# Optimization experiments

Hardware: AMD Instinct MI355X
Metric: run time of the kernel (lower is better)

The kernel has to match this reference:

```python
import jax, jax.numpy as jnp
import numpy as np

EPS_BN = 1e-5   # torch BatchNorm1d default eps
EPS_L1 = 1e-9   # offset-attention renorm eps


def batchnorm(x, g, b):
    # training-mode BN over (batch, points) per channel; x: [B, C, N]
    mu = x.mean(axis=(0, 2), keepdims=True)
    var = x.var(axis=(0, 2), keepdims=True)  # biased, matching torch normalization
    return g[None, :, None] * (x - mu) * jax.lax.rsqrt(var + EPS_BN) + b[None, :, None]


def sub_ie(x, Wqk, Wv, bv, Wt, bt, g, b):
    # x: [B, C, N]; Wqk: [C//4, C] (q_conv and k_conv share weights)
    q = jnp.einsum('dc,bcn->bdn', Wqk, x)                    # [B, C/4, N]
    energy = jnp.einsum('bdi,bdj->bij', q, q)                # [B, N, N] symmetric Gram
    att = jax.nn.softmax(energy, axis=-1)                    # softmax over keys (dim=-1)
    att = att / (EPS_L1 + att.sum(axis=1, keepdims=True))    # extra L1 renorm over queries (dim=1)
    v = jnp.einsum('dc,bcn->bdn', Wv, x) + bv[None, :, None]  # [B, C, N]
    x_r = jnp.einsum('bci,bij->bcj', v, att)                 # bmm(x_v, attention)
    y = jnp.einsum('dc,bcn->bdn', Wt, x - x_r) + bt[None, :, None]
    y = jax.nn.relu(batchnorm(y, g, b))
    return x + y


def setup_inputs() -> dict:
    key = jax.random.key(0)
    ks = jax.random.split(key, 8)
    B, Cin, C, N = 8, 64, 128, 2048
    s = lambda k, shape: jax.random.normal(k, shape, jnp.float32) * 0.05
    return {
        'x':   jax.random.normal(ks[0], (B, Cin, N), jnp.float32),
        'W1':  s(ks[1], (64, 64)),
        'g1':  jnp.ones(64, jnp.float32),  'b1': jnp.zeros(64, jnp.float32),
        'W2':  s(ks[2], (C, 64)),
        'g2':  jnp.ones(C, jnp.float32),   'b2': jnp.zeros(C, jnp.float32),
        'Wqk': s(ks[3], (4, C // 4, C)),
        'Wv':  s(ks[4], (4, C, C)),        'bv': jnp.zeros((4, C), jnp.float32),
        'Wt':  s(ks[5], (4, C, C)),        'bt': jnp.zeros((4, C), jnp.float32),
        'gn':  jnp.ones((4, C), jnp.float32), 'bnb': jnp.zeros((4, C), jnp.float32),
    }


def reference(x, W1, g1, b1, W2, g2, b2, Wqk, Wv, bv, Wt, bt, gn, bnb):
    h = jax.nn.relu(batchnorm(jnp.einsum('dc,bcn->bdn', W1, x), g1, b1))   # [B,64,N]
    h = jax.nn.relu(batchnorm(jnp.einsum('dc,bcn->bdn', W2, h), g2, b2))   # [B,128,N]
    outs = []
    for i in range(4):  # 4 structurally chained offset-attention blocks
        h = sub_ie(h, Wqk[i], Wv[i], bv[i], Wt[i], bt[i], gn[i], bnb[i])
        outs.append(h)
    return jnp.concatenate(outs, axis=1)  # [B, 512, N]
```

## Files before the change

### kernel.cpp

```cpp
#include <hip/hip_runtime.h>
#include <cstdint>
#include <cstddef>

#define NPTS 2048
#define NBAT 8

typedef unsigned long long ull;
typedef __attribute__((ext_vector_type(8))) short bf16x8;
typedef __attribute__((ext_vector_type(4))) float f32x4;

__device__ __forceinline__ float4 ld4(const float* p){ return *reinterpret_cast<const float4*>(p); }
__device__ __forceinline__ void st4(float* p, float4 v){ *reinterpret_cast<float4*>(p) = v; }
__device__ __forceinline__ unsigned short f2bf(float f){
    unsigned int u = __float_as_uint(f);
    u += 0x7FFFu + ((u >> 16) & 1u);
    return (unsigned short)(u >> 16);
}
__device__ __forceinline__ float bf2f(unsigned short h){
    return __uint_as_float(((unsigned int)h) << 16);
}

typedef __attribute__((address_space(3))) unsigned int lds_u32;
typedef __attribute__((address_space(1))) const unsigned int glb_u32;
__device__ __forceinline__ void gl2lds16(const unsigned short* g, unsigned short* l){
    __builtin_amdgcn_global_load_lds((glb_u32*)g, (lds_u32*)l, 16, 0, 0);
}

__global__ __launch_bounds__(256) void zero_kernel(float* __restrict__ p)
{
    int i = (blockIdx.x * 256 + threadIdx.x) * 4;
    st4(&p[i], (float4){0.f, 0.f, 0.f, 0.f});
}

__device__ __forceinline__ void bn_finalize(const float* part, int C, int c,
                                            float& mean, float& istd)
{
    float s = 0.f, s2 = 0.f;
    #pragma unroll
    for (int b = 0; b < NBAT; ++b) {
        s  += part[b * C + c];
        s2 += part[NBAT * C + b * C + c];
    }
    const float invn = 1.f / (NBAT * NPTS);
    mean = s * invn;
    float var = s2 * invn - mean * mean;
    istd = rsqrtf(var + 1e-5f);
}

template<int CIN, int COUT, int TD, int TN, int MODE, bool BIAS, bool BNIN, bool STATS>
__global__ __launch_bounds__(256) void lin_mfma_kernel(
        const float* __restrict__ W, const float* __restrict__ X,
        const float* __restrict__ bias,
        const float* __restrict__ gin, const float* __restrict__ betain,
        const float* __restrict__ pin, float* __restrict__ pout,
        void* __restrict__ outv, void* __restrict__ outv2)
{
    constexpr int WD  = TD / 16;
    constexpr int NPW = TN * WD / 4;
    constexpr int FB  = NPW / 16;
    constexpr int KS  = CIN / 32;
    __shared__ unsigned short Xhi[TN * CIN];
    __shared__ unsigned short Xlo[TN * CIN];
    __shared__ float gaL[CIN];
    __shared__ float beL[CIN];
    const int tid = threadIdx.x;
    const int lane = tid & 63;
    const int w = tid >> 6;
    const int g = lane >> 4;
    const int l15 = lane & 15;
    const int b = blockIdx.z;
    const int d0 = blockIdx.y * TD;
    const int n0 = blockIdx.x * TN;
    const int dw = (w % WD) * 16;
    const int nw = (w / WD) * NPW;

    if (BNIN) {
        if (tid < CIN) {
            float mean, is;
            bn_finalize(pin, CIN, tid, mean, is);
            float ga = gin[tid] * is;
            gaL[tid] = ga;
            beL[tid] = betain[tid] - mean * ga;
        }
        __syncthreads();
    }

    bf16x8 Whi[KS], Wlo[KS];
    {
        const int d = d0 + dw + l15;
        #pragma unroll
        for (int ks = 0; ks < KS; ++ks) {
            float4 a = ld4(&W[(size_t)d * CIN + ks * 32 + g * 8]);
            float4 bq = ld4(&W[(size_t)d * CIN + ks * 32 + g * 8 + 4]);
            float vv[8] = {a.x, a.y, a.z, a.w, bq.x, bq.y, bq.z, bq.w};
            bf16x8 h8, l8;
            #pragma unroll
            for (int e = 0; e < 8; ++e) {
                unsigned short hh = f2bf(vv[e]);
                h8[e] = (short)hh;
                l8[e] = (short)f2bf(vv[e] - bf2f(hh));
            }
            Whi[ks] = h8; Wlo[ks] = l8;
        }
    }
    constexpr int TN4 = TN / 4;
    constexpr int NF = (TN * CIN) / 1024;
    #pragma unroll
    for (int f = 0; f < NF; ++f) {
        int idx = tid + 256 * f;
        int c = idx / TN4;
        int n = (idx % TN4) * 4;
        float4 xv = ld4(&X[((size_t)(b * CIN + c)) * NPTS + n0 + n]);
        float vv[4] = {xv.x, xv.y, xv.z, xv.w};
        if (BNIN) {
            float ga = gaL[c], be = beL[c];
            #pragma unroll
            for (int j2 = 0; j2 < 4; ++j2) vv[j2] = fmaxf(fmaf(ga, vv[j2], be), 0.f);
        }
        #pragma unroll
        for (int j2 = 0; j2 < 4; ++j2) {
            int nn = n + j2;
            int cp = (c + nn * 8) & (CIN - 1);
            unsigned short hh = f2bf(vv[j2]);
            Xhi[nn * CIN + cp] = hh;
            Xlo[nn * CIN + cp] = f2bf(vv[j2] - bf2f(hh));
        }
    }
    __syncthreads();

    f32x4 acc[FB];
    #pragma unroll
    for (int fb = 0; fb < FB; ++fb) acc[fb] = (f32x4){0.f, 0.f, 0.f, 0.f};
    #pragma unroll
    for (int ks = 0; ks < KS; ++ks) {
        #pragma unroll
        for (int fb = 0; fb < FB; ++fb) {
            int n = nw + fb * 16 + l15;
            int cp = (ks * 32 + g * 8 + n * 8) & (CIN - 1);
            bf16x8 xh = *reinterpret_cast<bf16x8*>(&Xhi[n * CIN + cp]);
            bf16x8 xl = *reinterpret_cast<bf16x8*>(&Xlo[n * CIN + cp]);
            acc[fb] = __builtin_amdgcn_mfma_f32_16x16x32_bf16(Wlo[ks], xh, acc[fb], 0, 0, 0);
            acc[fb] = __builtin_amdgcn_mfma_f32_16x16x32_bf16(Whi[ks], xl, acc[fb], 0, 0, 0);
            acc[fb] = __builtin_amdgcn_mfma_f32_16x16x32_bf16(Whi[ks], xh, acc[fb], 0, 0, 0);
        }
    }
    const int dbase = d0 + dw + g * 4;
    float bb[4] = {0.f, 0.f, 0.f, 0.f};
    if (BIAS) {
        float4 b4 = ld4(&bias[dbase]);
        bb[0] = b4.x; bb[1] = b4.y; bb[2] = b4.z; bb[3] = b4.w;
    }
    float s1[4] = {0.f, 0.f, 0.f, 0.f};
    float s2[4] = {0.f, 0.f, 0.f, 0.f};
    #pragma unroll
    for (int fb = 0; fb < FB; ++fb) {
        int ncol = n0 + nw + fb * 16 + l15;
        if (MODE == 2) {
            unsigned short* qh = (unsigned short*)outv;
            unsigned short* ql = (unsigned short*)outv2;
            ushort4 hh, ll;
            float q0 = acc[fb][0], q1 = acc[fb][1], q2 = acc[fb][2], q3 = acc[fb][3];
            hh.x = f2bf(q0); ll.x = f2bf(q0 - bf2f(hh.x));
            hh.y = f2bf(q1); ll.y = f2bf(q1 - bf2f(hh.y));
            hh.z = f2bf(q2); ll.z = f2bf(q2 - bf2f(hh.z));
            hh.w = f2bf(q3); ll.w = f2bf(q3 - bf2f(hh.w));
            *reinterpret_cast<ushort4*>(&qh[((size_t)b * NPTS + ncol) * 32 + dbase]) = hh;
            *reinterpret_cast<ushort4*>(&ql[((size_t)b * NPTS + ncol) * 32 + dbase]) = ll;
        } else if (MODE == 1) {
            unsigned short* ob = (unsigned short*)outv;
            #pragma unroll
            for (int r = 0; r < 4; ++r)
                ob[((size_t)(b * COUT + dbase + r)) * NPTS + ncol] = f2bf(acc[fb][r] + bb[r]);
        } else {
            float* ob = (float*)outv;
            #pragma unroll
            for (int r = 0; r < 4; ++r) {
                float val = acc[fb][r] + bb[r];
                ob[((size_t)(b * COUT + dbase + r)) * NPTS + ncol] = val;
                if (STATS) { s1[r] += val; s2[r] += val * val; }
            }
        }
    }
    if (STATS) {
        #pragma unroll
        for (int r = 0; r < 4; ++r) {
            float a1 = s1[r], a2 = s2[r];
            a1 += __shfl_xor(a1, 1, 64);  a2 += __shfl_xor(a2, 1, 64);
            a1 += __shfl_xor(a1, 2, 64);  a2 += __shfl_xor(a2, 2, 64);
            a1 += __shfl_xor(a1, 4, 64);  a2 += __shfl_xor(a2, 4, 64);
            a1 += __shfl_xor(a1, 8, 64);  a2 += __shfl_xor(a2, 8, 64);
            if (l15 == 0) {
                atomicAdd(&pout[b * COUT + dbase + r], a1);
                atomicAdd(&pout[NBAT * COUT + b * COUT + dbase + r], a2);
            }
        }
    }
}

__global__ __launch_bounds__(256) void rowstats_fused_kernel(
        const unsigned short* __restrict__ qThi, const unsigned short* __restrict__ qTlo,
        float* __restrict__ rowm, float* __restrict__ rowinv)
{
    __shared__ float pm[4][16];
    __shared__ float ps[4][16];
    const int lane = threadIdx.x & 63;
    const int w = threadIdx.x >> 6;
    const int b = blockIdx.y;
    const int i0 = blockIdx.x * 16;
    const int g = lane >> 4;
    const int l15 = lane & 15;
    const int iR = i0 + l15;
    const bf16x8 bhi = *reinterpret_cast<const bf16x8*>(&qThi[((size_t)b * NPTS + iR) * 32 + g * 8]);
    const bf16x8 blo = *reinterpret_cast<const bf16x8*>(&qTlo[((size_t)b * NPTS + iR) * 32 + g * 8]);
    float m = -1e30f, s = 0.f;
    for (int t = w * 32; t < w * 32 + 32; ++t) {
        int jr = t * 16 + l15;
        const bf16x8 ahi = *reinterpret_cast<const bf16x8*>(&qThi[((size_t)b * NPTS + jr) * 32 + g * 8]);
        const bf16x8 alo = *reinterpret_cast<const bf16x8*>(&qTlo[((size_t)b * NPTS + jr) * 32 + g * 8]);
        f32x4 e4 = {0.f, 0.f, 0.f, 0.f};
        e4 = __builtin_amdgcn_mfma_f32_16x16x32_bf16(alo, bhi, e4, 0, 0, 0);
        e4 = __builtin_amdgcn_mfma_f32_16x16x32_bf16(ahi, blo, e4, 0, 0, 0);
        e4 = __builtin_amdgcn_mfma_f32_16x16x32_bf16(ahi, bhi, e4, 0, 0, 0);
        float tm = fmaxf(fmaxf(e4[0], e4[1]), fmaxf(e4[2], e4[3]));
        float nm = fmaxf(m, tm);
        s *= __expf(m - nm);
        m = nm;
        s += __expf(e4[0] - m) + __expf(e4[1] - m) + __expf(e4[2] - m) + __expf(e4[3] - m);
    }
    #pragma unroll
    for (int o = 16; o <= 32; o <<= 1) {
        float om = __shfl_xor(m, o, 64);
        float os = __shfl_xor(s, o, 64);
        float nm = fmaxf(m, om);
        s = s * __expf(m - nm) + os * __expf(om - nm);
        m = nm;
    }
    if (lane < 16) { pm[w][l15] = m; ps[w][l15] = s; }
    __syncthreads();
    if (threadIdx.x < 16) {
        float m0 = pm[0][threadIdx.x], m1 = pm[1][threadIdx.x];
        float m2 = pm[2][threadIdx.x], m3 = pm[3][threadIdx.x];
        float mf = fmaxf(fmaxf(m0, m1), fmaxf(m2, m3));
        float sf = ps[0][threadIdx.x] * __expf(m0 - mf)
                 + ps[1][threadIdx.x] * __expf(m1 - mf)
                 + ps[2][threadIdx.x] * __expf(m2 - mf)
                 + ps[3][threadIdx.x] * __expf(m3 - mf);
        rowm[(size_t)b * NPTS + i0 + threadIdx.x] = mf;
        rowinv[(size_t)b * NPTS + i0 + threadIdx.x] = 1.f / sf;
    }
}

__global__ __launch_bounds__(512) void attn_fused_kernel(
        const unsigned short* __restrict__ qThi, const unsigned short* __restrict__ qTlo,
        const unsigned short* __restrict__ V,
        const float* __restrict__ rowm, const float* __restrict__ rowinv,
        const float* __restrict__ H, float* __restrict__ T)
{
    __shared__ unsigned short Alds[128 * 128];
    __shared__ unsigned short Blds[32 * 128];
    __shared__ float cparts[8][16];
    const int tid = threadIdx.x;
    const int b  = blockIdx.y;
    const int j0 = blockIdx.x * 32;
    const int lane = tid & 63;
    const int w = tid >> 6;
    const int g = lane >> 4;
    const int l15 = lane & 15;
    const int jsub = w & 1;
    const int jl = jsub * 16 + l15;
    const int cb = (w >> 1) * 32;
    const int jb = jsub * 16;
    const bf16x8 bhi = *reinterpret_cast<const bf16x8*>(&qThi[((size_t)b * NPTS + j0 + jl) * 32 + g * 8]);
    const bf16x8 blo = *reinterpret_cast<const bf16x8*>(&qTlo[((size_t)b * NPTS + j0 + jl) * 32 + g * 8]);
    f32x4 acc[2];
    acc[0] = (f32x4){0.f, 0.f, 0.f, 0.f};
    acc[1] = (f32x4){0.f, 0.f, 0.f, 0.f};
    float csum = 0.f;

    for (int i0 = 0; i0 < NPTS; i0 += 128) {
        __syncthreads();
        #pragma unroll
        for (int t = 0; t < 4; ++t) {
            int c = w * 16 + t * 4 + g;
            int s = l15;
            int slot = (s & 8) | ((s & 7) ^ (c & 7));
            gl2lds16(V + ((size_t)(b * 128 + c)) * NPTS + i0 + slot * 8,
                     &Alds[(w * 16 + t * 4) * 128]);
        }
        #pragma unroll
        for (int half = 0; half < 2; ++half) {
            int it = (w >> 1) + half * 4;
            int iA = i0 + it * 16 + l15;
            const bf16x8 ahi = *reinterpret_cast<const bf16x8*>(&qThi[((size_t)b * NPTS + iA) * 32 + g * 8]);
            const bf16x8 alo = *reinterpret_cast<const bf16x8*>(&qTlo[((size_t)b * NPTS + iA) * 32 + g * 8]);
            f32x4 e4 = {0.f, 0.f, 0.f, 0.f};
            e4 = __builtin_amdgcn_mfma_f32_16x16x32_bf16(alo, bhi, e4, 0, 0, 0);
            e4 = __builtin_amdgcn_mfma_f32_16x16x32_bf16(ahi, blo, e4, 0, 0, 0);
            e4 = __builtin_amdgcn_mfma_f32_16x16x32_bf16(ahi, bhi, e4, 0, 0, 0);
            int ibase = i0 + it * 16 + g * 4;
            float4 mv = ld4(&rowm[(size_t)b * NPTS + ibase]);
            float4 sv = ld4(&rowinv[(size_t)b * NPTS + ibase]);
            float p0 = __expf(e4[0] - mv.x) * sv.x;
            float p1 = __expf(e4[1] - mv.y) * sv.y;
            float p2 = __expf(e4[2] - mv.z) * sv.z;
            float p3 = __expf(e4[3] - mv.w) * sv.w;
            csum += p0 + p1 + p2 + p3;
            int il = it * 16 + g * 4;
            int slot = il >> 3;
            int sl = (slot & 8) | ((slot & 7) ^ (jl & 7));
            ull pk = (ull)f2bf(p0) | ((ull)f2bf(p1) << 16) |
                     ((ull)f2bf(p2) << 32) | ((ull)f2bf(p3) << 48);
            *reinterpret_cast<ull*>(&Blds[jl * 128 + sl * 8 + (il & 7)]) = pk;
        }
        __syncthreads();
        #pragma unroll
        for (int ks = 0; ks < 4; ++ks) {
            int j = jb + l15;
            int slot = ks * 4 + g;
            int slb = (slot & 8) | ((slot & 7) ^ (j & 7));
            bf16x8 bfr = *reinterpret_cast<bf16x8*>(&Blds[j * 128 + slb * 8]);
            #pragma unroll
            for (int fa = 0; fa < 2; ++fa) {
                int c = cb + fa * 16 + l15;
                int sla = (slot & 8) | ((slot & 7) ^ (c & 7));
                bf16x8 afr = *reinterpret_cast<bf16x8*>(&Alds[c * 128 + sla * 8]);
                acc[fa] = __builtin_amdgcn_mfma_f32_16x16x32_bf16(afr, bfr, acc[fa], 0, 0, 0);
            }
        }
    }
    csum += __shfl_xor(csum, 16, 64);
    csum += __shfl_xor(csum, 32, 64);
    if (lane < 16) cparts[w][l15] = csum;
    __syncthreads();
    float cs = cparts[jsub][l15] + cparts[jsub + 2][l15]
             + cparts[jsub + 4][l15] + cparts[jsub + 6][l15];
    float inv = 1.f / (1e-9f + cs);
    int jg_ = j0 + jb + l15;
    #pragma unroll
    for (int fa = 0; fa < 2; ++fa) {
        #pragma unroll
        for (int r = 0; r < 4; ++r) {
            int c = cb + fa * 16 + g * 4 + r;
            size_t base = ((size_t)(b * 128 + c)) * NPTS + jg_;
            T[base] = H[base] - acc[fa][r] * inv;
        }
    }
}

__global__ __launch_bounds__(256) void bn_apply_kernel(const float* __restrict__ X,
        const float* __restrict__ g, const float* __restrict__ beta,
        const float* __restrict__ part, int C, float* __restrict__ out)
{
    const int bc = blockIdx.y;
    const int c = bc % C;
    const int n = blockIdx.x * 1024 + threadIdx.x * 4;
    float mean, is;
    bn_finalize(part, C, c, mean, is);
    const float ga = g[c] * is;
    const float be = beta[c] - mean * ga;
    float4 v = ld4(&X[(size_t)bc * NPTS + n]);
    float4 o;
    o.x = fmaxf(fmaf(ga, v.x, be), 0.f);
    o.y = fmaxf(fmaf(ga, v.y, be), 0.f);
    o.z = fmaxf(fmaf(ga, v.z, be), 0.f);
    o.w = fmaxf(fmaf(ga, v.w, be), 0.f);
    st4(&out[(size_t)bc * NPTS + n], o);
}

__global__ __launch_bounds__(256) void bn_res_kernel(const float* __restrict__ Y,
        const float* __restrict__ g, const float* __restrict__ beta,
        const float* __restrict__ part, float* __restrict__ H,
        float* __restrict__ out, int blk)
{
    const int bc = blockIdx.y;
    const int c = bc & 127;
    const int b = bc >> 7;
    const int n = blockIdx.x * 1024 + threadIdx.x * 4;
    float mean, is;
    bn_finalize(part, 128, c, mean, is);
    const float ga = g[c] * is;
    const float be = beta[c] - mean * ga;
    float4 yv = ld4(&Y[(size_t)bc * NPTS + n]);
    float4 hv = ld4(&H[(size_t)bc * NPTS + n]);
    float4 o;
    o.x = hv.x + fmaxf(fmaf(ga, yv.x, be), 0.f);
    o.y = hv.y + fmaxf(fmaf(ga, yv.y, be), 0.f);
    o.z = hv.z + fmaxf(fmaf(ga, yv.z, be), 0.f);
    o.w = hv.w + fmaxf(fmaf(ga, yv.w, be), 0.f);
    st4(&H[(size_t)bc * NPTS + n], o);
    st4(&out[((size_t)(b * 512 + blk * 128 + c)) * NPTS + n], o);
}

extern "C" void kernel_launch(void* const* d_in, const int* in_sizes, int n_in,
                              void* d_out, int out_size, void* d_ws, size_t ws_size,
                              hipStream_t stream)
{
    const float* x   = (const float*)d_in[0];
    const float* W1  = (const float*)d_in[1];
    const float* g1  = (const float*)d_in[2];
    const float* b1  = (const float*)d_in[3];
    const float* W2  = (const float*)d_in[4];
    const float* g2  = (const float*)d_in[5];
    const float* b2  = (const float*)d_in[6];
    const float* Wqk = (const float*)d_in[7];
    const float* Wv  = (const float*)d_in[8];
    const float* bv  = (const float*)d_in[9];
    const float* Wt  = (const float*)d_in[10];
    const float* bt  = (const float*)d_in[11];
    const float* gn  = (const float*)d_in[12];
    const float* bnb = (const float*)d_in[13];
    float* out = (float*)d_out;

    float* ws = (float*)d_ws;
    size_t off = 0;
    auto alloc = [&](size_t n) { float* p = ws + off; off += n; return p; };
    float* h      = alloc((size_t)NBAT * 128 * NPTS);
    float* t      = alloc((size_t)NBAT * 128 * NPTS);
    float* y      = alloc((size_t)NBAT * 128 * NPTS);
    float* y2     = alloc((size_t)NBAT * 128 * NPTS);
    float* part   = alloc(6 * 2 * NBAT * 128);
    float* rowm   = alloc((size_t)NBAT * NPTS);
    float* rowinv = alloc((size_t)NBAT * NPTS);
    unsigned short* vb   = (unsigned short*)alloc((size_t)NBAT * 128 * NPTS / 2);
    unsigned short* qThi = (unsigned short*)alloc((size_t)NBAT * NPTS * 32 / 2);
    unsigned short* qTlo = (unsigned short*)alloc((size_t)NBAT * NPTS * 32 / 2);
    const int PSL = 2 * NBAT * 128;

    zero_kernel<<<12, 256, 0, stream>>>(part);

    lin_mfma_kernel<64, 64, 64, 32, 0, false, false, true>
        <<<dim3(64, 1, NBAT), 256, 0, stream>>>(
        W1, x, nullptr, nullptr, nullptr, nullptr, part + 0 * PSL, y, nullptr);
    lin_mfma_kernel<64, 128, 64, 32, 0, false, true, true>
        <<<dim3(64, 2, NBAT), 256, 0, stream>>>(
        W2, y, nullptr, g1, b1, part + 0 * PSL, part + 1 * PSL, y2, nullptr);
    bn_apply_kernel<<<dim3(2, NBAT * 128), 256, 0, stream>>>(
        y2, g2, b2, part + 1 * PSL, 128, h);

    for (int blk = 0; blk < 4; ++blk) {
        lin_mfma_kernel<128, 32, 32, 32, 2, false, false, false>
            <<<dim3(64, 1, NBAT), 256, 0, stream>>>(
            Wqk + (size_t)blk * 32 * 128, h, nullptr,
            nullptr, nullptr, nullptr, nullptr, qThi, qTlo);
        lin_mfma_kernel<128, 128, 64, 32, 1, true, false, false>
            <<<dim3(64, 2, NBAT), 256, 0, stream>>>(
            Wv + (size_t)blk * 128 * 128, h, bv + blk * 128,
            nullptr, nullptr, nullptr, nullptr, vb, nullptr);
        rowstats_fused_kernel<<<dim3(128, NBAT), 256, 0, stream>>>(qThi, qTlo, rowm, rowinv);
        attn_fused_kernel<<<dim3(64, NBAT), 512, 0, stream>>>(
            qThi, qTlo, vb, rowm, rowinv, h, t);
        lin_mfma_kernel<128, 128, 64, 32, 0, true, false, true>
            <<<dim3(64, 2, NBAT), 256, 0, stream>>>(
            Wt + (size_t)blk * 128 * 128, t, bt + blk * 128,
            nullptr, nullptr, nullptr, part + (2 + blk) * PSL, y, nullptr);
        bn_res_kernel<<<dim3(2, NBAT * 128), 256, 0, stream>>>(
            y, gn + blk * 128, bnb + blk * 128, part + (2 + blk) * PSL, h, out, blk);
    }
}
```

Measured before the change: 445.3 us.

## Double-buffer attention LDS tiles with register prefetch of next V and q chunk

Rewrites the fused attention loop to step over 64-point chunks instead of 128, with double-buffered LDS for the V and probability tiles. The next chunk's V, q hi/lo fragments and row stats are prefetched into registers while the current chunk computes, which removes one barrier per iteration. The async global_load_lds path is replaced by register loads followed by LDS stores. Register pressure rises, each MFMA stage gets shorter, and the number of loop iterations doubles.

```diff
diff --git a/kernel.cpp b/kernel.cpp
--- a/kernel.cpp
+++ b/kernel.cpp
@@ -18,12 +18,6 @@
 }
 __device__ __forceinline__ float bf2f(unsigned short h){
     return __uint_as_float(((unsigned int)h) << 16);
-}
-
-typedef __attribute__((address_space(3))) unsigned int lds_u32;
-typedef __attribute__((address_space(1))) const unsigned int glb_u32;
-__device__ __forceinline__ void gl2lds16(const unsigned short* g, unsigned short* l){
-    __builtin_amdgcn_global_load_lds((glb_u32*)g, (lds_u32*)l, 16, 0, 0);
 }
 
 __global__ __launch_bounds__(256) void zero_kernel(float* __restrict__ p)
@@ -256,8 +250,8 @@
         const float* __restrict__ rowm, const float* __restrict__ rowinv,
         const float* __restrict__ H, float* __restrict__ T)
 {
-    __shared__ unsigned short Alds[128 * 128];
-    __shared__ unsigned short Blds[32 * 128];
+    __shared__ unsigned short Alds[2][128 * 64];
+    __shared__ unsigned short Blds[2][32 * 64];
     __shared__ float cparts[8][16];
     const int tid = threadIdx.x;
     const int b  = blockIdx.y;
@@ -267,9 +261,12 @@
     const int g = lane >> 4;
     const int l15 = lane & 15;
     const int jsub = w & 1;
+    const int tE = w >> 1;
     const int jl = jsub * 16 + l15;
     const int cb = (w >> 1) * 32;
     const int jb = jsub * 16;
+    const int vc = tid >> 3, vslot = tid & 7;
+    const int vc1 = (tid + 512) >> 3, vslot1 = (tid + 512) & 7;
     const bf16x8 bhi = *reinterpret_cast<const bf16x8*>(&qThi[((size_t)b * NPTS + j0 + jl) * 32 + g * 8]);
     const bf16x8 blo = *reinterpret_cast<const bf16x8*>(&qTlo[((size_t)b * NPTS + j0 + jl) * 32 + g * 8]);
     f32x4 acc[2];
@@ -277,56 +274,61 @@
     acc[1] = (f32x4){0.f, 0.f, 0.f, 0.f};
     float csum = 0.f;
 
-    for (int i0 = 0; i0 < NPTS; i0 += 128) {
-        __syncthreads();
-        #pragma unroll
-        for (int t = 0; t < 4; ++t) {
-            int c = w * 16 + t * 4 + g;
-            int s = l15;
-            int slot = (s & 8) | ((s & 7) ^ (c & 7));
-            gl2lds16(V + ((size_t)(b * 128 + c)) * NPTS + i0 + slot * 8,
-                     &Alds[(w * 16 + t * 4) * 128]);
-        }
-        #pragma unroll
-        for (int half = 0; half < 2; ++half) {
-            int it = (w >> 1) + half * 4;
-            int iA = i0 + it * 16 + l15;
-            const bf16x8 ahi = *reinterpret_cast<const bf16x8*>(&qThi[((size_t)b * NPTS + iA) * 32 + g * 8]);
-            const bf16x8 alo = *reinterpret_cast<const bf16x8*>(&qTlo[((size_t)b * NPTS + iA) * 32 + g * 8]);
+    float4 vreg0 = ld4((const float*)(V + ((size_t)(b * 128 + vc)) * NPTS + vslot * 8));
+    float4 vreg1 = ld4((const float*)(V + ((size_t)(b * 128 + vc1)) * NPTS + vslot1 * 8));
+    bf16x8 pahi = *reinterpret_cast<const bf16x8*>(&qThi[((size_t)b * NPTS + tE * 16 + l15) * 32 + g * 8]);
+    bf16x8 palo = *reinterpret_cast<const bf16x8*>(&qTlo[((size_t)b * NPTS + tE * 16 + l15) * 32 + g * 8]);
+    float4 pmv = ld4(&rowm[(size_t)b * NPTS + tE * 16 + g * 4]);
+    float4 psv = ld4(&rowinv[(size_t)b * NPTS + tE * 16 + g * 4]);
+
+    int p = 0;
+    for (int i0 = 0; i0 < NPTS; i0 += 64) {
+        {
+            int sl = vslot ^ (vc & 7);
+            *reinterpret_cast<float4*>(&Alds[p][vc * 64 + sl * 8]) = vreg0;
+            sl = vslot1 ^ (vc1 & 7);
+            *reinterpret_cast<float4*>(&Alds[p][vc1 * 64 + sl * 8]) = vreg1;
+        }
+        {
             f32x4 e4 = {0.f, 0.f, 0.f, 0.f};
-            e4 = __builtin_amdgcn_mfma_f32_16x16x32_bf16(alo, bhi, e4, 0, 0, 0);
-            e4 = __builtin_amdgcn_mfma_f32_16x16x32_bf16(ahi, blo, e4, 0, 0, 0);
-            e4 = __builtin_amdgcn_mfma_f32_16x16x32_bf16(ahi, bhi, e4, 0, 0, 0);
-            int ibase = i0 + it * 16 + g * 4;
-            float4 mv = ld4(&rowm[(size_t)b * NPTS + ibase]);
-            float4 sv = ld4(&rowinv[(size_t)b * NPTS + ibase]);
-            float p0 = __expf(e4[0] - mv.x) * sv.x;
-            float p1 = __expf(e4[1] - mv.y) * sv.y;
-            float p2 = __expf(e4[2] - mv.z) * sv.z;
-            float p3 = __expf(e4[3] - mv.w) * sv.w;
+            e4 = __builtin_amdgcn_mfma_f32_16x16x32_bf16(palo, bhi, e4, 0, 0, 0);
+            e4 = __builtin_amdgcn_mfma_f32_16x16x32_bf16(pahi, blo, e4, 0, 0, 0);
+            e4 = __builtin_amdgcn_mfma_f32_16x16x32_bf16(pahi, bhi, e4, 0, 0, 0);
+            float p0 = __expf(e4[0] - pmv.x) * psv.x;
+            float p1 = __expf(e4[1] - pmv.y) * psv.y;
+            float p2 = __expf(e4[2] - pmv.z) * psv.z;
+            float p3 = __expf(e4[3] - pmv.w) * psv.w;
             csum += p0 + p1 + p2 + p3;
-            int il = it * 16 + g * 4;
-            int slot = il >> 3;
-            int sl = (slot & 8) | ((slot & 7) ^ (jl & 7));
+            int il = tE * 16 + g * 4;
+            int sl = (il >> 3) ^ (jl & 7);
             ull pk = (ull)f2bf(p0) | ((ull)f2bf(p1) << 16) |
                      ((ull)f2bf(p2) << 32) | ((ull)f2bf(p3) << 48);
-            *reinterpret_cast<ull*>(&Blds[jl * 128 + sl * 8 + (il & 7)]) = pk;
+            *reinterpret_cast<ull*>(&Blds[p][jl * 64 + sl * 8 + (il & 7)]) = pk;
+        }
+        {
+            int i0n = (i0 + 64) & (NPTS - 1);
+            vreg0 = ld4((const float*)(V + ((size_t)(b * 128 + vc)) * NPTS + i0n + vslot * 8));
+            vreg1 = ld4((const float*)(V + ((size_t)(b * 128 + vc1)) * NPTS + i0n + vslot1 * 8));
+            pahi = *reinterpret_cast<const bf16x8*>(&qThi[((size_t)b * NPTS + i0n + tE * 16 + l15) * 32 + g * 8]);
+            palo = *reinterpret_cast<const bf16x8*>(&qTlo[((size_t)b * NPTS + i0n + tE * 16 + l15) * 32 + g * 8]);
+            pmv = ld4(&rowm[(size_t)b * NPTS + i0n + tE * 16 + g * 4]);
+            psv = ld4(&rowinv[(size_t)b * NPTS + i0n + tE * 16 + g * 4]);
         }
         __syncthreads();
         #pragma unroll
-        for (int ks = 0; ks < 4; ++ks) {
+        for (int ks = 0; ks < 2; ++ks) {
             int j = jb + l15;
-            int slot = ks * 4 + g;
-            int slb = (slot & 8) | ((slot & 7) ^ (j & 7));
-            bf16x8 bfr = *reinterpret_cast<bf16x8*>(&Blds[j * 128 + slb * 8]);
+            int slb = (ks * 4 + g) ^ (j & 7);
+            bf16x8 bfr = *reinterpret_cast<bf16x8*>(&Blds[p][j * 64 + slb * 8]);
             #pragma unroll
             for (int fa = 0; fa < 2; ++fa) {
                 int c = cb + fa * 16 + l15;
-                int sla = (slot & 8) | ((slot & 7) ^ (c & 7));
-                bf16x8 afr = *reinterpret_cast<bf16x8*>(&Alds[c * 128 + sla * 8]);
+                int sla = (ks * 4 + g) ^ (c & 7);
+                bf16x8 afr = *reinterpret_cast<bf16x8*>(&Alds[p][c * 64 + sla * 8]);
                 acc[fa] = __builtin_amdgcn_mfma_f32_16x16x32_bf16(afr, bfr, acc[fa], 0, 0, 0);
             }
         }
+        p ^= 1;
     }
     csum += __shfl_xor(csum, 16, 64);
     csum += __shfl_xor(csum, 32, 64);
```

Result: faster. 402.4 us (-9.6%).
